# Performance work log

Measured on AMD Instinct MI355X. Metric: run time of the kernel, lower is better.

The kernel has to match this reference:

```python
import jax, jax.numpy as jnp
import numpy as np

N_NODES = 50000
N_EDGES = 800000
LEAKY_SLOPE = 0.01
DROPOUT_P = 0.5


def _graph_conv(src, dst, x, W, b):
    """DGL GraphConv with norm='both': D_out^{-1/2} A D_in^{-1/2} X W + b."""
    n = x.shape[0]
    ones = jnp.ones((src.shape[0],), dtype=x.dtype)
    deg_out = jax.ops.segment_sum(ones, src, num_segments=n)  # out-degree of src nodes
    deg_in = jax.ops.segment_sum(ones, dst, num_segments=n)   # in-degree of dst nodes
    norm_src = jax.lax.rsqrt(jnp.maximum(deg_out, 1.0))
    norm_dst = jax.lax.rsqrt(jnp.maximum(deg_in, 1.0))
    h = (x * norm_src[:, None]) @ W          # apply weight before aggregation
    agg = jax.ops.segment_sum(h[src], dst, num_segments=n)  # SpMM aggregate
    return agg * norm_dst[:, None] + b


def _dropout(x, key, p=DROPOUT_P):
    keep = jax.random.bernoulli(key, 1.0 - p, x.shape)
    return jnp.where(keep, x / (1.0 - p), jnp.zeros((), x.dtype))


def setup_inputs() -> dict:
    key = jax.random.key(0)
    ks = jax.random.split(key, 8)
    features = jax.random.normal(ks[0], (N_NODES, 128), dtype=jnp.float32)
    src = jax.random.randint(ks[1], (N_EDGES,), 0, N_NODES, dtype=jnp.int64)
    dst = jax.random.randint(ks[2], (N_EDGES,), 0, N_NODES, dtype=jnp.int64)
    s1 = 1.0 / np.sqrt(128.0)
    s3 = 1.0 / np.sqrt(128.0)
    W1 = jax.random.normal(ks[3], (128, 128), dtype=jnp.float32) * s1
    W2 = jax.random.normal(ks[4], (128, 128), dtype=jnp.float32) * s1
    W3 = jax.random.normal(ks[5], (128, 64), dtype=jnp.float32) * s3
    b1 = jnp.zeros((128,), dtype=jnp.float32)
    b2 = jnp.zeros((128,), dtype=jnp.float32)
    b3 = jnp.zeros((64,), dtype=jnp.float32)
    return {"features": features, "src": src, "dst": dst,
            "W1": W1, "b1": b1, "W2": W2, "b2": b2, "W3": W3, "b3": b3}


def reference(features, src, dst, W1, b1, W2, b2, W3, b3):
    dk = jax.random.split(jax.random.key(42), 3)
    h = jax.nn.leaky_relu(_graph_conv(src, dst, features, W1, b1), LEAKY_SLOPE)
    h = _dropout(h, dk[0])
    h = jax.nn.leaky_relu(_graph_conv(src, dst, h, W2, b2), LEAKY_SLOPE)
    h = _dropout(h, dk[1])
    h = jax.nn.leaky_relu(_graph_conv(src, dst, h, W3, b3), LEAKY_SLOPE)
    h = _dropout(h, dk[2])
    return h
```

## Files before the change

kernel.cpp:

```cpp
#include <hip/hip_runtime.h>
#include <stdint.h>

using short8 = __attribute__((ext_vector_type(8))) short;
using f32x4  = __attribute__((ext_vector_type(4))) float;

#define SLOT_CAP 64
#define LDW 136
#define NBINS 50176
#define LWORDS 12544
#define NCHUNK 128

#define TFR(r) { x0 += x1; x1 = (x1 << r) | (x1 >> (32 - r)); x1 ^= x0; }

__host__ __device__ inline void threefry2x32(uint32_t k0, uint32_t k1,
                                             uint32_t c0, uint32_t c1,
                                             uint32_t& o0, uint32_t& o1) {
  uint32_t ks2 = k0 ^ k1 ^ 0x1BD11BDAu;
  uint32_t x0 = c0 + k0, x1 = c1 + k1;
  TFR(13) TFR(15) TFR(26) TFR(6)  x0 += k1;  x1 += ks2 + 1u;
  TFR(17) TFR(29) TFR(16) TFR(24) x0 += ks2; x1 += k0 + 2u;
  TFR(13) TFR(15) TFR(26) TFR(6)  x0 += k0;  x1 += k1 + 3u;
  TFR(17) TFR(29) TFR(16) TFR(24) x0 += k1;  x1 += ks2 + 4u;
  TFR(13) TFR(15) TFR(26) TFR(6)  x0 += ks2; x1 += k0 + 5u;
  o0 = x0; o1 = x1;
}

__device__ inline float tf_uniform(uint32_t k0, uint32_t k1, uint32_t i) {
  uint32_t o0, o1;
  threefry2x32(k0, k1, 0u, i, o0, o1);
  uint32_t bits = o0 ^ o1;
  return __uint_as_float((bits >> 9) | 0x3F800000u) - 1.0f;
}

__device__ inline uint16_t f2bf(float f) {
  uint32_t u = __float_as_uint(f);
  return (uint16_t)((u + 0x7FFFu + ((u >> 16) & 1u)) >> 16);
}
__device__ inline uint32_t pack2bf(float a, float b) {
  return (uint32_t)f2bf(a) | ((uint32_t)f2bf(b) << 16);
}
__device__ inline float bflo(uint32_t w) { return __uint_as_float(w << 16); }
__device__ inline float bfhi(uint32_t w) { return __uint_as_float(w & 0xFFFF0000u); }

__global__ __launch_bounds__(256) void build_hist_kernel(
    const int* __restrict__ src, const int* __restrict__ dst,
    uint16_t* __restrict__ histD, uint16_t* __restrict__ histS,
    const float* __restrict__ W1, const float* __restrict__ W2,
    const float* __restrict__ W3, uint16_t* __restrict__ Wt,
    int n, int nE, int HR, int EPB) {
  const int bid = (int)blockIdx.x;
  if (bid >= 512) {
    int i = (bid - 512) * 256 + (int)threadIdx.x;
    float v;
    if (i < 16384) {
      int nr = i >> 7, k = i & 127;
      v = W1[k * 128 + nr];
    } else if (i < 32768) {
      int j = i - 16384, nr = j >> 7, k = j & 127;
      v = W2[k * 128 + nr];
    } else if (i < 40960) {
      int j = i - 32768, nr = j >> 7, k = j & 127;
      v = W3[k * 64 + nr];
    } else return;
    Wt[i] = f2bf(v);
    return;
  }

  __shared__ uint32_t bins[LWORDS];
  const bool isSrc = bid >= 256;
  const int c = bid & 127;
  const int h = (bid >> 7) & 1;
  const int lo = h * HR;
  const int* keys = isSrc ? src : dst;
  uint16_t* hist = isSrc ? histS : histD;

  for (int i = threadIdx.x; i < LWORDS; i += 256) bins[i] = 0u;
  __syncthreads();

  const int e0 = c * EPB, e1 = min(e0 + EPB, nE);
  for (int e = e0 + (int)threadIdx.x; e < e1; e += 256) {
    int k = keys[e] - lo;
    if ((unsigned)k < (unsigned)HR)
      atomicAdd(&bins[k >> 1], 1u << ((k & 1) * 16));
  }
  __syncthreads();

  uint32_t* out = (uint32_t*)(hist + (size_t)c * NBINS + lo);
  const int wlim = (min(HR, n - lo) + 1) >> 1;
  for (int i = threadIdx.x; i < wlim; i += 256) out[i] = bins[i];
}

__global__ __launch_bounds__(256) void reduce_kernel(
    uint16_t* __restrict__ histD, const uint16_t* __restrict__ histS,
    int* __restrict__ degin, float* __restrict__ nsrc, int n) {
  const int v = blockIdx.x * 256 + (int)threadIdx.x;
  if (v >= n) return;
  uint32_t run = 0;
  #pragma unroll 4
  for (int c = 0; c < NCHUNK; ++c) {
    size_t idx = (size_t)c * NBINS + v;
    uint16_t x = histD[idx];
    histD[idx] = (uint16_t)run;
    run += x;
  }
  degin[v] = (int)run;
  uint32_t s = 0;
  #pragma unroll 4
  for (int c = 0; c < NCHUNK; ++c) s += histS[(size_t)c * NBINS + v];
  nsrc[v] = rsqrtf(fmaxf((float)s, 1.0f));
}

__global__ __launch_bounds__(256) void scatter_build_kernel(
    const int* __restrict__ src, const int* __restrict__ dst,
    const uint16_t* __restrict__ cumD, uint16_t* __restrict__ edge_slots,
    int nE, int HR, int EPB) {
  __shared__ uint32_t bins[LWORDS];
  const int c = (int)blockIdx.x & 127;
  const int h = ((int)blockIdx.x >> 7) & 1;
  const int lo = h * HR;

  for (int i = threadIdx.x; i < LWORDS; i += 256) bins[i] = 0u;
  __syncthreads();

  const int e0 = c * EPB, e1 = min(e0 + EPB, nE);
  for (int e = e0 + (int)threadIdx.x; e < e1; e += 256) {
    int d = dst[e];
    int k = d - lo;
    if ((unsigned)k < (unsigned)HR) {
      uint32_t old = atomicAdd(&bins[k >> 1], 1u << ((k & 1) * 16));
      int rank = (int)((old >> ((k & 1) * 16)) & 0xFFFFu);
      int pos = (int)cumD[(size_t)c * NBINS + d] + rank;
      if (pos < SLOT_CAP) edge_slots[((size_t)d << 6) + pos] = (uint16_t)src[e];
    }
  }
}

__global__ __launch_bounds__(256) void gemm1_kernel(
    const float* __restrict__ X, const float* __restrict__ nsrc,
    const uint16_t* __restrict__ Wt1, uint16_t* __restrict__ h1, int n) {
  const int r0 = (int)blockIdx.x * 64;
  const int tid = (int)threadIdx.x;
  const int wave = tid >> 6, lane = tid & 63;
  const int wm = wave & 1, wn = wave >> 1;
  const int lane15 = lane & 15, quad = lane >> 4;

  const int rowA0 = r0 + wm * 32 + lane15;
  const int rowA1 = rowA0 + 16;
  const bool v0 = rowA0 < n, v1 = rowA1 < n;

  f32x4 acc[2][4] = {};
  #pragma unroll
  for (int kc = 0; kc < 128; kc += 32) {
    const int ko = kc + quad * 8;
    union { short8 s; uint32_t u[4]; } a0, a1;
    a0.u[0] = a0.u[1] = a0.u[2] = a0.u[3] = 0u;
    a1.u[0] = a1.u[1] = a1.u[2] = a1.u[3] = 0u;
    if (v0) {
      float4 x0 = *(const float4*)&X[(size_t)rowA0 * 128 + ko];
      float4 x1 = *(const float4*)&X[(size_t)rowA0 * 128 + ko + 4];
      a0.u[0] = pack2bf(x0.x, x0.y); a0.u[1] = pack2bf(x0.z, x0.w);
      a0.u[2] = pack2bf(x1.x, x1.y); a0.u[3] = pack2bf(x1.z, x1.w);
    }
    if (v1) {
      float4 x0 = *(const float4*)&X[(size_t)rowA1 * 128 + ko];
      float4 x1 = *(const float4*)&X[(size_t)rowA1 * 128 + ko + 4];
      a1.u[0] = pack2bf(x0.x, x0.y); a1.u[1] = pack2bf(x0.z, x0.w);
      a1.u[2] = pack2bf(x1.x, x1.y); a1.u[3] = pack2bf(x1.z, x1.w);
    }
    #pragma unroll
    for (int nt = 0; nt < 4; ++nt) {
      int nn = wn * 64 + nt * 16 + lane15;
      short8 b = *(const short8*)&Wt1[nn * 128 + ko];
      acc[0][nt] = __builtin_amdgcn_mfma_f32_16x16x32_bf16(a0.s, b, acc[0][nt], 0, 0, 0);
      acc[1][nt] = __builtin_amdgcn_mfma_f32_16x16x32_bf16(a1.s, b, acc[1][nt], 0, 0, 0);
    }
  }

  #pragma unroll
  for (int mt = 0; mt < 2; ++mt) {
    #pragma unroll
    for (int reg = 0; reg < 4; ++reg) {
      int row = r0 + wm * 32 + mt * 16 + quad * 4 + reg;
      if (row < n) {
        float nsr = nsrc[row];
        #pragma unroll
        for (int nt = 0; nt < 4; ++nt) {
          int col = wn * 64 + nt * 16 + lane15;
          h1[(size_t)row * 128 + col] = f2bf(acc[mt][nt][reg] * nsr);
        }
      }
    }
  }
}

template<int NCOLS>
__global__ __launch_bounds__(256) void fuse_gather_gemm_kernel(
    const uint16_t* __restrict__ h_in, const int* __restrict__ degin,
    const uint16_t* __restrict__ edge_slots, const float* __restrict__ nsrc,
    const float* __restrict__ bias, const uint16_t* __restrict__ Wt,
    uint16_t* __restrict__ h_out, uint32_t k0, uint32_t k1, int n) {
  __shared__ uint16_t Xs[64 * LDW];
  __shared__ float ns_s[64];
  const int r0 = (int)blockIdx.x * 64;
  const int tid = (int)threadIdx.x;

  if (tid < 64) {
    int row = r0 + tid;
    ns_s[tid] = (row < n) ? nsrc[row] : 1.0f;
  }

  #pragma unroll
  for (int it = 0; it < 4; ++it) {
    const int nl = it * 16 + tid / 16;
    const int node = r0 + nl;
    const int c8 = (tid & 15) * 8;

    if (node < n) {
      float acc[8] = {0.f, 0.f, 0.f, 0.f, 0.f, 0.f, 0.f, 0.f};
      const int dgi = degin[node];
      const int deg = min(dgi, SLOT_CAP);
      const uint16_t* slots = edge_slots + ((size_t)node << 6);
      const uint16_t* hb = h_in + c8;

      int e = 0;
      for (; e + 4 <= deg; e += 4) {
        uint64_t sl = *(const uint64_t*)&slots[e];
        int s0 = (int)(sl & 0xFFFF), s1 = (int)((sl >> 16) & 0xFFFF);
        int s2 = (int)((sl >> 32) & 0xFFFF), s3 = (int)(sl >> 48);
        uint4 r0v = *(const uint4*)(hb + (size_t)s0 * 128);
        uint4 r1v = *(const uint4*)(hb + (size_t)s1 * 128);
        uint4 r2v = *(const uint4*)(hb + (size_t)s2 * 128);
        uint4 r3v = *(const uint4*)(hb + (size_t)s3 * 128);
        acc[0] += bflo(r0v.x) + bflo(r1v.x) + bflo(r2v.x) + bflo(r3v.x);
        acc[1] += bfhi(r0v.x) + bfhi(r1v.x) + bfhi(r2v.x) + bfhi(r3v.x);
        acc[2] += bflo(r0v.y) + bflo(r1v.y) + bflo(r2v.y) + bflo(r3v.y);
        acc[3] += bfhi(r0v.y) + bfhi(r1v.y) + bfhi(r2v.y) + bfhi(r3v.y);
        acc[4] += bflo(r0v.z) + bflo(r1v.z) + bflo(r2v.z) + bflo(r3v.z);
        acc[5] += bfhi(r0v.z) + bfhi(r1v.z) + bfhi(r2v.z) + bfhi(r3v.z);
        acc[6] += bflo(r0v.w) + bflo(r1v.w) + bflo(r2v.w) + bflo(r3v.w);
        acc[7] += bfhi(r0v.w) + bfhi(r1v.w) + bfhi(r2v.w) + bfhi(r3v.w);
      }
      for (; e < deg; ++e) {
        uint4 r = *(const uint4*)(hb + (size_t)slots[e] * 128);
        acc[0] += bflo(r.x); acc[1] += bfhi(r.x);
        acc[2] += bflo(r.y); acc[3] += bfhi(r.y);
        acc[4] += bflo(r.z); acc[5] += bfhi(r.z);
        acc[6] += bflo(r.w); acc[7] += bfhi(r.w);
      }

      const float nd = rsqrtf(fmaxf((float)dgi, 1.0f));
      const float4 b0 = *(const float4*)&bias[c8];
      const float4 b1 = *(const float4*)&bias[c8 + 4];
      const float bb[8] = {b0.x, b0.y, b0.z, b0.w, b1.x, b1.y, b1.z, b1.w};
      const uint32_t i0 = (uint32_t)(node * 128 + c8);

      float o[8];
      #pragma unroll
      for (int j = 0; j < 8; ++j) {
        float v = acc[j] * nd + bb[j];
        v = (v >= 0.f) ? v : 0.01f * v;
        o[j] = (tf_uniform(k0, k1, i0 + (uint32_t)j) < 0.5f) ? v * 2.0f : 0.0f;
      }

      uint4 w;
      w.x = pack2bf(o[0], o[1]); w.y = pack2bf(o[2], o[3]);
      w.z = pack2bf(o[4], o[5]); w.w = pack2bf(o[6], o[7]);
      *(uint4*)&Xs[nl * LDW + c8] = w;
    } else {
      *(uint4*)&Xs[nl * LDW + c8] = make_uint4(0u, 0u, 0u, 0u);
    }
  }
  __syncthreads();

  const int wave = tid >> 6, lane = tid & 63;
  const int wm = wave & 1, wn = wave >> 1;
  const int lane15 = lane & 15, quad = lane >> 4;
  constexpr int NT = NCOLS / 32;

  f32x4 acc[2][NT] = {};
  #pragma unroll
  for (int kc = 0; kc < 128; kc += 32) {
    const int ko = kc + quad * 8;
    short8 a0 = *(const short8*)&Xs[(wm * 32 + lane15) * LDW + ko];
    short8 a1 = *(const short8*)&Xs[(wm * 32 + 16 + lane15) * LDW + ko];
    #pragma unroll
    for (int nt = 0; nt < NT; ++nt) {
      int nn = wn * (NCOLS / 2) + nt * 16 + lane15;
      short8 b = *(const short8*)&Wt[nn * 128 + ko];
      acc[0][nt] = __builtin_amdgcn_mfma_f32_16x16x32_bf16(a0, b, acc[0][nt], 0, 0, 0);
      acc[1][nt] = __builtin_amdgcn_mfma_f32_16x16x32_bf16(a1, b, acc[1][nt], 0, 0, 0);
    }
  }

  #pragma unroll
  for (int mt = 0; mt < 2; ++mt) {
    #pragma unroll
    for (int nt = 0; nt < NT; ++nt) {
      #pragma unroll
      for (int reg = 0; reg < 4; ++reg) {
        int rl = wm * 32 + mt * 16 + quad * 4 + reg;
        int row = r0 + rl;
        if (row < n) {
          int col = wn * (NCOLS / 2) + nt * 16 + lane15;
          h_out[(size_t)row * NCOLS + col] = f2bf(acc[mt][nt][reg] * ns_s[rl]);
        }
      }
    }
  }
}

__global__ __launch_bounds__(256) void gather_out_kernel(
    const uint16_t* __restrict__ h3, const int* __restrict__ degin,
    const uint16_t* __restrict__ edge_slots, const float* __restrict__ bias,
    float* __restrict__ out, uint32_t k0, uint32_t k1, int n) {
  const int node = (int)blockIdx.x * 32 + (int)(threadIdx.x >> 3);
  if (node >= n) return;
  const int c8 = (threadIdx.x & 7) * 8;

  const int dgi = degin[node];
  const int deg = min(dgi, SLOT_CAP);
  const uint16_t* slots = edge_slots + ((size_t)node << 6);
  const uint16_t* hb = h3 + c8;

  float acc[8] = {0.f, 0.f, 0.f, 0.f, 0.f, 0.f, 0.f, 0.f};
  int e = 0;
  for (; e + 4 <= deg; e += 4) {
    uint64_t sl = *(const uint64_t*)&slots[e];
    int s0 = (int)(sl & 0xFFFF), s1 = (int)((sl >> 16) & 0xFFFF);
    int s2 = (int)((sl >> 32) & 0xFFFF), s3 = (int)(sl >> 48);
    uint4 r0 = *(const uint4*)(hb + (size_t)s0 * 64);
    uint4 r1 = *(const uint4*)(hb + (size_t)s1 * 64);
    uint4 r2 = *(const uint4*)(hb + (size_t)s2 * 64);
    uint4 r3 = *(const uint4*)(hb + (size_t)s3 * 64);
    acc[0] += bflo(r0.x) + bflo(r1.x) + bflo(r2.x) + bflo(r3.x);
    acc[1] += bfhi(r0.x) + bfhi(r1.x) + bfhi(r2.x) + bfhi(r3.x);
    acc[2] += bflo(r0.y) + bflo(r1.y) + bflo(r2.y) + bflo(r3.y);
    acc[3] += bfhi(r0.y) + bfhi(r1.y) + bfhi(r2.y) + bfhi(r3.y);
    acc[4] += bflo(r0.z) + bflo(r1.z) + bflo(r2.z) + bflo(r3.z);
    acc[5] += bfhi(r0.z) + bfhi(r1.z) + bfhi(r2.z) + bfhi(r3.z);
    acc[6] += bflo(r0.w) + bflo(r1.w) + bflo(r2.w) + bflo(r3.w);
    acc[7] += bfhi(r0.w) + bfhi(r1.w) + bfhi(r2.w) + bfhi(r3.w);
  }
  for (; e < deg; ++e) {
    uint4 r = *(const uint4*)(hb + (size_t)slots[e] * 64);
    acc[0] += bflo(r.x); acc[1] += bfhi(r.x);
    acc[2] += bflo(r.y); acc[3] += bfhi(r.y);
    acc[4] += bflo(r.z); acc[5] += bfhi(r.z);
    acc[6] += bflo(r.w); acc[7] += bfhi(r.w);
  }

  const float nd = rsqrtf(fmaxf((float)dgi, 1.0f));
  const float4 b0 = *(const float4*)&bias[c8];
  const float4 b1 = *(const float4*)&bias[c8 + 4];
  const float bb[8] = {b0.x, b0.y, b0.z, b0.w, b1.x, b1.y, b1.z, b1.w};
  const uint32_t i0 = (uint32_t)(node * 64 + c8);

  float o[8];
  #pragma unroll
  for (int j = 0; j < 8; ++j) {
    float v = acc[j] * nd + bb[j];
    v = (v >= 0.f) ? v : 0.01f * v;
    o[j] = (tf_uniform(k0, k1, i0 + (uint32_t)j) < 0.5f) ? v * 2.0f : 0.0f;
  }

  float* op = &out[(size_t)node * 64 + c8];
  *(float4*)op = make_float4(o[0], o[1], o[2], o[3]);
  *(float4*)(op + 4) = make_float4(o[4], o[5], o[6], o[7]);
}

extern "C" void kernel_launch(void* const* d_in, const int* in_sizes, int n_in,
                              void* d_out, int out_size, void* d_ws, size_t ws_size,
                              hipStream_t stream) {
  const float* features = (const float*)d_in[0];
  const int*   src      = (const int*)d_in[1];
  const int*   dst      = (const int*)d_in[2];
  const float* W1       = (const float*)d_in[3];
  const float* b1       = (const float*)d_in[4];
  const float* W2       = (const float*)d_in[5];
  const float* b2       = (const float*)d_in[6];
  const float* W3       = (const float*)d_in[7];
  const float* b3       = (const float*)d_in[8];
  float* out = (float*)d_out;

  const int n  = in_sizes[0] / 128;
  const int nE = in_sizes[1];

  char* p = (char*)d_ws;
  uint16_t* histD      = (uint16_t*)p; p += (size_t)NCHUNK * NBINS * 2;
  uint16_t* histS      = (uint16_t*)p; p += (size_t)NCHUNK * NBINS * 2;
  int* degin           = (int*)p;      p += (size_t)n * 4;
  float* nsrc          = (float*)p;    p += (size_t)n * 4;
  uint16_t* edge_slots = (uint16_t*)p; p += (size_t)n * SLOT_CAP * 2;
  uint16_t* Wt         = (uint16_t*)p; p += 40960 * 2;
  uint16_t* h1         = (uint16_t*)p; p += (size_t)n * 128 * 2;
  uint16_t* h2         = (uint16_t*)p; p += (size_t)n * 128 * 2;
  uint16_t* h3         = (uint16_t*)p;

  uint32_t dk[3][2];
  for (uint32_t i = 0; i < 3; ++i)
    threefry2x32(0u, 42u, 0u, i, dk[i][0], dk[i][1]);

  const int EPB = (nE + NCHUNK - 1) / NCHUNK;
  int HR = ((n + 3) / 2) & ~1;
  if (HR > 2 * LWORDS) HR = 2 * LWORDS;
  const int gb = (n + 63) / 64;

  build_hist_kernel<<<672, 256, 0, stream>>>(src, dst, histD, histS,
                                             W1, W2, W3, Wt, n, nE, HR, EPB);
  reduce_kernel<<<(n + 255) / 256, 256, 0, stream>>>(histD, histS, degin, nsrc, n);
  scatter_build_kernel<<<256, 256, 0, stream>>>(src, dst, histD, edge_slots,
                                                nE, HR, EPB);
  gemm1_kernel<<<gb, 256, 0, stream>>>(features, nsrc, Wt, h1, n);
  fuse_gather_gemm_kernel<128><<<gb, 256, 0, stream>>>(
      h1, degin, edge_slots, nsrc, b1, Wt + 16384, h2, dk[0][0], dk[0][1], n);
  fuse_gather_gemm_kernel<64><<<gb, 256, 0, stream>>>(
      h2, degin, edge_slots, nsrc, b2, Wt + 32768, h3, dk[1][0], dk[1][1], n);
  gather_out_kernel<<<(n + 31) / 32, 256, 0, stream>>>(
      h3, degin, edge_slots, b3, out, dk[2][0], dk[2][1], n);
}
```

Baseline: 278.5 us.

## Merge scatter with gemm1, halve gather tile rows, widen gather per-thread loads

The edge-slot scatter and the first GEMM are merged into one launch. Blocks below 256 do the scatter and the rest compute h1, since the two are independent. This removes one kernel launch and lets the two run concurrently. The fused gather+GEMM kernel now handles 32 rows per block, with each thread gathering 16 columns (two 16-byte loads per edge). This doubles the grid size and halves the MFMA work per wave. The output gather now takes 8 slot indices per 16-byte load. The trade-offs are higher register pressure per thread, and the merged kernel carries the scatter's large shared-memory footprint for its GEMM blocks too, which may limit occupancy.

```diff
diff --git a/kernel.cpp b/kernel.cpp
--- a/kernel.cpp
+++ b/kernel.cpp
@@ -41,6 +41,13 @@
 }
 __device__ inline float bflo(uint32_t w) { return __uint_as_float(w << 16); }
 __device__ inline float bfhi(uint32_t w) { return __uint_as_float(w & 0xFFFF0000u); }
+
+__device__ inline void acc8(float* a, uint4 r) {
+  a[0] += bflo(r.x); a[1] += bfhi(r.x);
+  a[2] += bflo(r.y); a[3] += bfhi(r.y);
+  a[4] += bflo(r.z); a[5] += bfhi(r.z);
+  a[6] += bflo(r.w); a[7] += bfhi(r.w);
+}
 
 __global__ __launch_bounds__(256) void build_hist_kernel(
     const int* __restrict__ src, const int* __restrict__ dst,
@@ -110,35 +117,38 @@
   nsrc[v] = rsqrtf(fmaxf((float)s, 1.0f));
 }
 
-__global__ __launch_bounds__(256) void scatter_build_kernel(
+__global__ __launch_bounds__(256) void scatter_gemm1_kernel(
     const int* __restrict__ src, const int* __restrict__ dst,
     const uint16_t* __restrict__ cumD, uint16_t* __restrict__ edge_slots,
-    int nE, int HR, int EPB) {
+    const float* __restrict__ X, const float* __restrict__ nsrc,
+    const uint16_t* __restrict__ Wt1, uint16_t* __restrict__ h1,
+    int n, int nE, int HR, int EPB) {
   __shared__ uint32_t bins[LWORDS];
-  const int c = (int)blockIdx.x & 127;
-  const int h = ((int)blockIdx.x >> 7) & 1;
-  const int lo = h * HR;
-
-  for (int i = threadIdx.x; i < LWORDS; i += 256) bins[i] = 0u;
-  __syncthreads();
-
-  const int e0 = c * EPB, e1 = min(e0 + EPB, nE);
-  for (int e = e0 + (int)threadIdx.x; e < e1; e += 256) {
-    int d = dst[e];
-    int k = d - lo;
-    if ((unsigned)k < (unsigned)HR) {
-      uint32_t old = atomicAdd(&bins[k >> 1], 1u << ((k & 1) * 16));
-      int rank = (int)((old >> ((k & 1) * 16)) & 0xFFFFu);
-      int pos = (int)cumD[(size_t)c * NBINS + d] + rank;
-      if (pos < SLOT_CAP) edge_slots[((size_t)d << 6) + pos] = (uint16_t)src[e];
-    }
-  }
-}
-
-__global__ __launch_bounds__(256) void gemm1_kernel(
-    const float* __restrict__ X, const float* __restrict__ nsrc,
-    const uint16_t* __restrict__ Wt1, uint16_t* __restrict__ h1, int n) {
-  const int r0 = (int)blockIdx.x * 64;
+  const int bid = (int)blockIdx.x;
+
+  if (bid < 256) {
+    const int c = bid & 127;
+    const int h = (bid >> 7) & 1;
+    const int lo = h * HR;
+
+    for (int i = threadIdx.x; i < LWORDS; i += 256) bins[i] = 0u;
+    __syncthreads();
+
+    const int e0 = c * EPB, e1 = min(e0 + EPB, nE);
+    for (int e = e0 + (int)threadIdx.x; e < e1; e += 256) {
+      int d = dst[e];
+      int k = d - lo;
+      if ((unsigned)k < (unsigned)HR) {
+        uint32_t old = atomicAdd(&bins[k >> 1], 1u << ((k & 1) * 16));
+        int rank = (int)((old >> ((k & 1) * 16)) & 0xFFFFu);
+        int pos = (int)cumD[(size_t)c * NBINS + d] + rank;
+        if (pos < SLOT_CAP) edge_slots[((size_t)d << 6) + pos] = (uint16_t)src[e];
+      }
+    }
+    return;
+  }
+
+  const int r0 = (bid - 256) * 64;
   const int tid = (int)threadIdx.x;
   const int wave = tid >> 6, lane = tid & 63;
   const int wm = wave & 1, wn = wave >> 1;
@@ -199,76 +209,80 @@
     const uint16_t* __restrict__ edge_slots, const float* __restrict__ nsrc,
     const float* __restrict__ bias, const uint16_t* __restrict__ Wt,
     uint16_t* __restrict__ h_out, uint32_t k0, uint32_t k1, int n) {
-  __shared__ uint16_t Xs[64 * LDW];
-  __shared__ float ns_s[64];
-  const int r0 = (int)blockIdx.x * 64;
+  __shared__ uint16_t Xs[32 * LDW];
+  __shared__ float ns_s[32];
+  const int r0 = (int)blockIdx.x * 32;
   const int tid = (int)threadIdx.x;
 
-  if (tid < 64) {
+  if (tid < 32) {
     int row = r0 + tid;
     ns_s[tid] = (row < n) ? nsrc[row] : 1.0f;
   }
 
-  #pragma unroll
-  for (int it = 0; it < 4; ++it) {
-    const int nl = it * 16 + tid / 16;
-    const int node = r0 + nl;
-    const int c8 = (tid & 15) * 8;
-
-    if (node < n) {
-      float acc[8] = {0.f, 0.f, 0.f, 0.f, 0.f, 0.f, 0.f, 0.f};
-      const int dgi = degin[node];
-      const int deg = min(dgi, SLOT_CAP);
-      const uint16_t* slots = edge_slots + ((size_t)node << 6);
-      const uint16_t* hb = h_in + c8;
-
-      int e = 0;
-      for (; e + 4 <= deg; e += 4) {
-        uint64_t sl = *(const uint64_t*)&slots[e];
-        int s0 = (int)(sl & 0xFFFF), s1 = (int)((sl >> 16) & 0xFFFF);
-        int s2 = (int)((sl >> 32) & 0xFFFF), s3 = (int)(sl >> 48);
-        uint4 r0v = *(const uint4*)(hb + (size_t)s0 * 128);
-        uint4 r1v = *(const uint4*)(hb + (size_t)s1 * 128);
-        uint4 r2v = *(const uint4*)(hb + (size_t)s2 * 128);
-        uint4 r3v = *(const uint4*)(hb + (size_t)s3 * 128);
-        acc[0] += bflo(r0v.x) + bflo(r1v.x) + bflo(r2v.x) + bflo(r3v.x);
-        acc[1] += bfhi(r0v.x) + bfhi(r1v.x) + bfhi(r2v.x) + bfhi(r3v.x);
-        acc[2] += bflo(r0v.y) + bflo(r1v.y) + bflo(r2v.y) + bflo(r3v.y);
-        acc[3] += bfhi(r0v.y) + bfhi(r1v.y) + bfhi(r2v.y) + bfhi(r3v.y);
-        acc[4] += bflo(r0v.z) + bflo(r1v.z) + bflo(r2v.z) + bflo(r3v.z);
-        acc[5] += bfhi(r0v.z) + bfhi(r1v.z) + bfhi(r2v.z) + bfhi(r3v.z);
-        acc[6] += bflo(r0v.w) + bflo(r1v.w) + bflo(r2v.w) + bflo(r3v.w);
-        acc[7] += bfhi(r0v.w) + bfhi(r1v.w) + bfhi(r2v.w) + bfhi(r3v.w);
-      }
-      for (; e < deg; ++e) {
-        uint4 r = *(const uint4*)(hb + (size_t)slots[e] * 128);
-        acc[0] += bflo(r.x); acc[1] += bfhi(r.x);
-        acc[2] += bflo(r.y); acc[3] += bfhi(r.y);
-        acc[4] += bflo(r.z); acc[5] += bfhi(r.z);
-        acc[6] += bflo(r.w); acc[7] += bfhi(r.w);
-      }
-
-      const float nd = rsqrtf(fmaxf((float)dgi, 1.0f));
-      const float4 b0 = *(const float4*)&bias[c8];
-      const float4 b1 = *(const float4*)&bias[c8 + 4];
-      const float bb[8] = {b0.x, b0.y, b0.z, b0.w, b1.x, b1.y, b1.z, b1.w};
-      const uint32_t i0 = (uint32_t)(node * 128 + c8);
-
-      float o[8];
-      #pragma unroll
-      for (int j = 0; j < 8; ++j) {
-        float v = acc[j] * nd + bb[j];
-        v = (v >= 0.f) ? v : 0.01f * v;
-        o[j] = (tf_uniform(k0, k1, i0 + (uint32_t)j) < 0.5f) ? v * 2.0f : 0.0f;
-      }
-
-      uint4 w;
-      w.x = pack2bf(o[0], o[1]); w.y = pack2bf(o[2], o[3]);
-      w.z = pack2bf(o[4], o[5]); w.w = pack2bf(o[6], o[7]);
-      *(uint4*)&Xs[nl * LDW + c8] = w;
-    } else {
-      *(uint4*)&Xs[nl * LDW + c8] = make_uint4(0u, 0u, 0u, 0u);
-    }
+  const int nl = tid >> 3;
+  const int node = r0 + nl;
+  const int c16 = (tid & 7) * 16;
+
+  if (node < n) {
+    float acc[16];
+    #pragma unroll
+    for (int j = 0; j < 16; ++j) acc[j] = 0.f;
+
+    const int dgi = degin[node];
+    const int deg = min(dgi, SLOT_CAP);
+    const uint16_t* slots = edge_slots + ((size_t)node << 6);
+    const uint16_t* hb = h_in + c16;
+
+    int e = 0;
+    for (; e + 4 <= deg; e += 4) {
+      uint64_t sl = *(const uint64_t*)&slots[e];
+      const uint16_t* p0 = hb + ((size_t)(sl & 0xFFFF) << 7);
+      const uint16_t* p1 = hb + ((size_t)((sl >> 16) & 0xFFFF) << 7);
+      const uint16_t* p2 = hb + ((size_t)((sl >> 32) & 0xFFFF) << 7);
+      const uint16_t* p3 = hb + ((size_t)(sl >> 48) << 7);
+      uint4 a0 = *(const uint4*)p0, b0 = *(const uint4*)(p0 + 8);
+      uint4 a1 = *(const uint4*)p1, b1 = *(const uint4*)(p1 + 8);
+      uint4 a2 = *(const uint4*)p2, b2 = *(const uint4*)(p2 + 8);
+      uint4 a3 = *(const uint4*)p3, b3 = *(const uint4*)(p3 + 8);
+      acc8(acc, a0); acc8(acc + 8, b0);
+      acc8(acc, a1); acc8(acc + 8, b1);
+      acc8(acc, a2); acc8(acc + 8, b2);
+      acc8(acc, a3); acc8(acc + 8, b3);
+    }
+    for (; e < deg; ++e) {
+      const uint16_t* pr = hb + ((size_t)slots[e] << 7);
+      uint4 ra = *(const uint4*)pr, rb = *(const uint4*)(pr + 8);
+      acc8(acc, ra); acc8(acc + 8, rb);
+    }
+
+    const float nd = rsqrtf(fmaxf((float)dgi, 1.0f));
+    const float4 b0 = *(const float4*)&bias[c16];
+    const float4 b1 = *(const float4*)&bias[c16 + 4];
+    const float4 b2 = *(const float4*)&bias[c16 + 8];
+    const float4 b3 = *(const float4*)&bias[c16 + 12];
+    const float bb[16] = {b0.x, b0.y, b0.z, b0.w, b1.x, b1.y, b1.z, b1.w,
+                          b2.x, b2.y, b2.z, b2.w, b3.x, b3.y, b3.z, b3.w};
+    const uint32_t i0 = (uint32_t)(node * 128 + c16);
+
+    float o[16];
+    #pragma unroll
+    for (int j = 0; j < 16; ++j) {
+      float v = acc[j] * nd + bb[j];
+      v = (v >= 0.f) ? v : 0.01f * v;
+      o[j] = (tf_uniform(k0, k1, i0 + (uint32_t)j) < 0.5f) ? v * 2.0f : 0.0f;
+    }
+
+    uint4 w0, w1;
+    w0.x = pack2bf(o[0], o[1]);   w0.y = pack2bf(o[2], o[3]);
+    w0.z = pack2bf(o[4], o[5]);   w0.w = pack2bf(o[6], o[7]);
+    w1.x = pack2bf(o[8], o[9]);   w1.y = pack2bf(o[10], o[11]);
+    w1.z = pack2bf(o[12], o[13]); w1.w = pack2bf(o[14], o[15]);
+    *(uint4*)&Xs[nl * LDW + c16] = w0;
+    *(uint4*)&Xs[nl * LDW + c16 + 8] = w1;
+  } else {
+    uint4 z = make_uint4(0u, 0u, 0u, 0u);
+    *(uint4*)&Xs[nl * LDW + c16] = z;
+    *(uint4*)&Xs[nl * LDW + c16 + 8] = z;
   }
   __syncthreads();
 
@@ -277,33 +291,28 @@
   const int lane15 = lane & 15, quad = lane >> 4;
   constexpr int NT = NCOLS / 32;
 
-  f32x4 acc[2][NT] = {};
+  f32x4 acc[NT] = {};
   #pragma unroll
   for (int kc = 0; kc < 128; kc += 32) {
     const int ko = kc + quad * 8;
-    short8 a0 = *(const short8*)&Xs[(wm * 32 + lane15) * LDW + ko];
-    short8 a1 = *(const short8*)&Xs[(wm * 32 + 16 + lane15) * LDW + ko];
+    short8 a = *(const short8*)&Xs[(wm * 16 + lane15) * LDW + ko];
     #pragma unroll
     for (int nt = 0; nt < NT; ++nt) {
       int nn = wn * (NCOLS / 2) + nt * 16 + lane15;
       short8 b = *(const short8*)&Wt[nn * 128 + ko];
-      acc[0][nt] = __builtin_amdgcn_mfma_f32_16x16x32_bf16(a0, b, acc[0][nt], 0, 0, 0);
-      acc[1][nt] = __builtin_amdgcn_mfma_f32_16x16x32_bf16(a1, b, acc[1][nt], 0, 0, 0);
+      acc[nt] = __builtin_amdgcn_mfma_f32_16x16x32_bf16(a, b, acc[nt], 0, 0, 0);
     }
   }
 
   #pragma unroll
-  for (int mt = 0; mt < 2; ++mt) {
-    #pragma unroll
-    for (int nt = 0; nt < NT; ++nt) {
-      #pragma unroll
-      for (int reg = 0; reg < 4; ++reg) {
-        int rl = wm * 32 + mt * 16 + quad * 4 + reg;
-        int row = r0 + rl;
-        if (row < n) {
-          int col = wn * (NCOLS / 2) + nt * 16 + lane15;
-          h_out[(size_t)row * NCOLS + col] = f2bf(acc[mt][nt][reg] * ns_s[rl]);
-        }
+  for (int nt = 0; nt < NT; ++nt) {
+    #pragma unroll
+    for (int reg = 0; reg < 4; ++reg) {
+      int rl = wm * 16 + quad * 4 + reg;
+      int row = r0 + rl;
+      if (row < n) {
+        int col = wn * (NCOLS / 2) + nt * 16 + lane15;
+        h_out[(size_t)row * NCOLS + col] = f2bf(acc[nt][reg] * ns_s[rl]);
       }
     }
   }
@@ -324,29 +333,22 @@
 
   float acc[8] = {0.f, 0.f, 0.f, 0.f, 0.f, 0.f, 0.f, 0.f};
   int e = 0;
-  for (; e + 4 <= deg; e += 4) {
-    uint64_t sl = *(const uint64_t*)&slots[e];
-    int s0 = (int)(sl & 0xFFFF), s1 = (int)((sl >> 16) & 0xFFFF);
-    int s2 = (int)((sl >> 32) & 0xFFFF), s3 = (int)(sl >> 48);
-    uint4 r0 = *(const uint4*)(hb + (size_t)s0 * 64);
-    uint4 r1 = *(const uint4*)(hb + (size_t)s1 * 64);
-    uint4 r2 = *(const uint4*)(hb + (size_t)s2 * 64);
-    uint4 r3 = *(const uint4*)(hb + (size_t)s3 * 64);
-    acc[0] += bflo(r0.x) + bflo(r1.x) + bflo(r2.x) + bflo(r3.x);
-    acc[1] += bfhi(r0.x) + bfhi(r1.x) + bfhi(r2.x) + bfhi(r3.x);
-    acc[2] += bflo(r0.y) + bflo(r1.y) + bflo(r2.y) + bflo(r3.y);
-    acc[3] += bfhi(r0.y) + bfhi(r1.y) + bfhi(r2.y) + bfhi(r3.y);
-    acc[4] += bflo(r0.z) + bflo(r1.z) + bflo(r2.z) + bflo(r3.z);
-    acc[5] += bfhi(r0.z) + bfhi(r1.z) + bfhi(r2.z) + bfhi(r3.z);
-    acc[6] += bflo(r0.w) + bflo(r1.w) + bflo(r2.w) + bflo(r3.w);
-    acc[7] += bfhi(r0.w) + bfhi(r1.w) + bfhi(r2.w) + bfhi(r3.w);
+  for (; e + 8 <= deg; e += 8) {
+    uint4 sl = *(const uint4*)&slots[e];
+    uint4 r0 = *(const uint4*)(hb + ((size_t)(sl.x & 0xFFFF) << 6));
+    uint4 r1 = *(const uint4*)(hb + ((size_t)(sl.x >> 16) << 6));
+    uint4 r2 = *(const uint4*)(hb + ((size_t)(sl.y & 0xFFFF) << 6));
+    uint4 r3 = *(const uint4*)(hb + ((size_t)(sl.y >> 16) << 6));
+    uint4 r4 = *(const uint4*)(hb + ((size_t)(sl.z & 0xFFFF) << 6));
+    uint4 r5 = *(const uint4*)(hb + ((size_t)(sl.z >> 16) << 6));
+    uint4 r6 = *(const uint4*)(hb + ((size_t)(sl.w & 0xFFFF) << 6));
+    uint4 r7 = *(const uint4*)(hb + ((size_t)(sl.w >> 16) << 6));
+    acc8(acc, r0); acc8(acc, r1); acc8(acc, r2); acc8(acc, r3);
+    acc8(acc, r4); acc8(acc, r5); acc8(acc, r6); acc8(acc, r7);
   }
   for (; e < deg; ++e) {
-    uint4 r = *(const uint4*)(hb + (size_t)slots[e] * 64);
-    acc[0] += bflo(r.x); acc[1] += bfhi(r.x);
-    acc[2] += bflo(r.y); acc[3] += bfhi(r.y);
-    acc[4] += bflo(r.z); acc[5] += bfhi(r.z);
-    acc[6] += bflo(r.w); acc[7] += bfhi(r.w);
+    uint4 r = *(const uint4*)(hb + ((size_t)slots[e] << 6));
+    acc8(acc, r);
   }
 
   const float nd = rsqrtf(fmaxf((float)dgi, 1.0f));
@@ -403,17 +405,17 @@
   const int EPB = (nE + NCHUNK - 1) / NCHUNK;
   int HR = ((n + 3) / 2) & ~1;
   if (HR > 2 * LWORDS) HR = 2 * LWORDS;
-  const int gb = (n + 63) / 64;
+  const int gb64 = (n + 63) / 64;
+  const int gb32 = (n + 31) / 32;
 
   build_hist_kernel<<<672, 256, 0, stream>>>(src, dst, histD, histS,
                                              W1, W2, W3, Wt, n, nE, HR, EPB);
   reduce_kernel<<<(n + 255) / 256, 256, 0, stream>>>(histD, histS, degin, nsrc, n);
-  scatter_build_kernel<<<256, 256, 0, stream>>>(src, dst, histD, edge_slots,
-                                                nE, HR, EPB);
-  gemm1_kernel<<<gb, 256, 0, stream>>>(features, nsrc, Wt, h1, n);
-  fuse_gather_gemm_kernel<128><<<gb, 256, 0, stream>>>(
+  scatter_gemm1_kernel<<<256 + gb64, 256, 0, stream>>>(
+      src, dst, histD, edge_slots, features, nsrc, Wt, h1, n, nE, HR, EPB);
+  fuse_gather_gemm_kernel<128><<<gb32, 256, 0, stream>>>(
       h1, degin, edge_slots, nsrc, b1, Wt + 16384, h2, dk[0][0], dk[0][1], n);
-  fuse_gather_gemm_kernel<64><<<gb, 256, 0, stream>>>(
+  fuse_gather_gemm_kernel<64><<<gb32, 256, 0, stream>>>(
       h2, degin, edge_slots, nsrc, b2, Wt + 32768, h3, dk[1][0], dk[1][1], n);
   gather_out_kernel<<<(n + 31) / 32, 256, 0, stream>>>(
       h3, degin, edge_slots, b3, out, dk[2][0], dk[2][1], n);
```

New measurement: 267.0 us. 1.04x faster.
